# Performance work log

Hardware: AMD Instinct MI355X
Metric: run time of the kernel (lower is better)

The kernel has to match this reference:

```python
import jax, jax.numpy as jnp
import numpy as np


def setup_inputs() -> dict:
    key = jax.random.key(0)
    k1, k2, k3, k4, k5 = jax.random.split(key, 5)
    B, Tx, Ty, E, D = 8, 256, 256, 256, 256
    return {
        "encoder_out_seq": jax.random.normal(k1, (B, Tx, E), dtype=jnp.float32),
        "decoder_out_seq": jax.random.normal(k2, (B, Ty, D), dtype=jnp.float32),
        "W_a": jax.random.normal(k3, (E, E), dtype=jnp.float32) * 0.05,
        "U_a": jax.random.normal(k4, (D, E), dtype=jnp.float32) * 0.05,
        "V_a": jax.random.normal(k5, (E, 1), dtype=jnp.float32) * 0.05,
    }


def reference(encoder_out_seq, decoder_out_seq, W_a, U_a, V_a):
    # encoder_out_seq: [B, Tx, E], decoder_out_seq: [B, Ty, D]
    # Vectorized Bahdanau additive attention (the K.rnn scan is a fake
    # recurrence: each timestep only uses the per-step decoder input and the
    # constant encoder sequence).
    W_dot_s = jnp.einsum("bxe,ef->bxf", encoder_out_seq, W_a)   # [B, Tx, E]
    U_dot_h = jnp.einsum("byd,de->bye", decoder_out_seq, U_a)   # [B, Ty, E]
    # [B, Ty, Tx, E] broadcast add + tanh, then project with V_a -> [B, Ty, Tx]
    Ws_plus_Uh = jnp.tanh(W_dot_s[:, None, :, :] + U_dot_h[:, :, None, :])
    e = jnp.einsum("byxe,eo->byx", Ws_plus_Uh, V_a)             # [B, Ty, Tx]
    e = jax.nn.softmax(e, axis=-1)                               # softmax over Tx
    # context: weighted sum of encoder states -> [B, Ty, E]
    c = jnp.einsum("byx,bxe->bye", e, encoder_out_seq)
    return (c, e)
```

## Files before the change

### kernel.cpp

```cpp
#include <hip/hip_runtime.h>
#include <cstddef>
#include <stdint.h>

#define NB 8
#define TX 256
#define TY 256
#define NE 256

#define CSC 2.8853900817779268f

__global__ __launch_bounds__(512) void prep_kernel(
    const float* __restrict__ enc, const float* __restrict__ dec,
    const float* __restrict__ Wa, const float* __restrict__ Ua,
    float* __restrict__ ZwT, float* __restrict__ Zu)
{
    const int tx = threadIdx.x;
    const int w  = threadIdx.y;
    const int tid = w * 64 + tx;
    int blk = blockIdx.x;
    const bool isU = blk >= 128;
    if (isU) blk -= 128;
    const int b  = blk >> 4;
    const int r0 = (blk & 15) * 16;

    __shared__ float rowsL[16 * NE];
    __shared__ float tL[16][260];

    const float* src = (isU ? dec : enc) + ((size_t)b * 256 + r0) * NE;
    ((float4*)rowsL)[tid]       = ((const float4*)src)[tid];
    ((float4*)rowsL)[tid + 512] = ((const float4*)src)[tid + 512];
    __syncthreads();

    const float* M = isU ? Ua : Wa;
    const int e0 = tx * 4;
    const int rA = w * 2, rB = w * 2 + 1;
    float4 acc0 = make_float4(0.f, 0.f, 0.f, 0.f);
    float4 acc1 = make_float4(0.f, 0.f, 0.f, 0.f);
    const float* rowA = rowsL + rA * NE;
    const float* rowB = rowsL + rB * NE;

    for (int k = 0; k < NE; k += 8) {
        float4 mw[8];
        #pragma unroll
        for (int j = 0; j < 8; ++j)
            mw[j] = *(const float4*)(M + (size_t)(k + j) * NE + e0);
        #pragma unroll
        for (int j = 0; j < 8; ++j) {
            const float a = rowA[k + j];
            const float c = rowB[k + j];
            acc0.x = __builtin_fmaf(a, mw[j].x, acc0.x);
            acc0.y = __builtin_fmaf(a, mw[j].y, acc0.y);
            acc0.z = __builtin_fmaf(a, mw[j].z, acc0.z);
            acc0.w = __builtin_fmaf(a, mw[j].w, acc0.w);
            acc1.x = __builtin_fmaf(c, mw[j].x, acc1.x);
            acc1.y = __builtin_fmaf(c, mw[j].y, acc1.y);
            acc1.z = __builtin_fmaf(c, mw[j].z, acc1.z);
            acc1.w = __builtin_fmaf(c, mw[j].w, acc1.w);
        }
    }
    acc0.x = __builtin_amdgcn_exp2f(acc0.x * CSC);
    acc0.y = __builtin_amdgcn_exp2f(acc0.y * CSC);
    acc0.z = __builtin_amdgcn_exp2f(acc0.z * CSC);
    acc0.w = __builtin_amdgcn_exp2f(acc0.w * CSC);
    acc1.x = __builtin_amdgcn_exp2f(acc1.x * CSC);
    acc1.y = __builtin_amdgcn_exp2f(acc1.y * CSC);
    acc1.z = __builtin_amdgcn_exp2f(acc1.z * CSC);
    acc1.w = __builtin_amdgcn_exp2f(acc1.w * CSC);

    if (isU) {
        *(float4*)(Zu + ((size_t)b * TY + r0 + rA) * NE + e0) = acc0;
        *(float4*)(Zu + ((size_t)b * TY + r0 + rB) * NE + e0) = acc1;
    } else {
        *(float4*)&tL[rA][e0] = acc0;
        *(float4*)&tL[rB][e0] = acc1;
        __syncthreads();
        #pragma unroll
        for (int rep = 0; rep < 2; ++rep) {
            const int f4id = tid + rep * 512;
            const int e  = f4id >> 2;
            const int xq = (f4id & 3) * 4;
            float4 o;
            o.x = tL[xq + 0][e];
            o.y = tL[xq + 1][e];
            o.z = tL[xq + 2][e];
            o.w = tL[xq + 3][e];
            *(float4*)(ZwT + (size_t)b * NE * TX + (size_t)e * TX + r0 + xq) = o;
        }
    }
}

__global__ __launch_bounds__(512, 4) void attn_kernel(
    const float* __restrict__ enc, const float* __restrict__ ZwT,
    const float* __restrict__ Zu, const float* __restrict__ Va,
    float* __restrict__ c_out, float* __restrict__ e_out)
{
    const int tx = threadIdx.x;
    const int w  = threadIdx.y;
    const int tid = w * 64 + tx;
    const int b  = blockIdx.x & 7;
    const int y0 = (blockIdx.x >> 3) * 4;

    __shared__ float4 zu4L[NE];
    __shared__ float  vL[NE];
    __shared__ float4 accL[8][4][64];
    __shared__ float  pL4[TX][4];

    {
        const int e = tid & 255;
        if (tid < 256) {
            const float* zp = Zu + ((size_t)b * TY + y0) * NE + e;
            zu4L[e] = make_float4(zp[0], zp[NE], zp[2 * NE], zp[3 * NE]);
        } else {
            vL[e] = Va[e];
        }
    }
    __syncthreads();

    const float* wp = ZwT + (size_t)b * NE * TX + (size_t)(w * 32) * TX + tx * 4;
    const float4* zup = &zu4L[w * 32];
    const float*  vp  = &vL[w * 32];
    float4 acc0 = make_float4(0.f, 0.f, 0.f, 0.f);
    float4 acc1 = acc0, acc2 = acc0, acc3 = acc0;
    #pragma unroll 4
    for (int e = 0; e < 32; ++e) {
        const float4 zw  = *(const float4*)(wp + (size_t)e * TX);
        const float4 zu4 = zup[e];
        const float  v   = vp[e];
        acc0.x = __builtin_fmaf(v, __builtin_amdgcn_rcpf(__builtin_fmaf(zw.x, zu4.x, 1.f)), acc0.x);
        acc0.y = __builtin_fmaf(v, __builtin_amdgcn_rcpf(__builtin_fmaf(zw.y, zu4.x, 1.f)), acc0.y);
        acc0.z = __builtin_fmaf(v, __builtin_amdgcn_rcpf(__builtin_fmaf(zw.z, zu4.x, 1.f)), acc0.z);
        acc0.w = __builtin_fmaf(v, __builtin_amdgcn_rcpf(__builtin_fmaf(zw.w, zu4.x, 1.f)), acc0.w);
        acc1.x = __builtin_fmaf(v, __builtin_amdgcn_rcpf(__builtin_fmaf(zw.x, zu4.y, 1.f)), acc1.x);
        acc1.y = __builtin_fmaf(v, __builtin_amdgcn_rcpf(__builtin_fmaf(zw.y, zu4.y, 1.f)), acc1.y);
        acc1.z = __builtin_fmaf(v, __builtin_amdgcn_rcpf(__builtin_fmaf(zw.z, zu4.y, 1.f)), acc1.z);
        acc1.w = __builtin_fmaf(v, __builtin_amdgcn_rcpf(__builtin_fmaf(zw.w, zu4.y, 1.f)), acc1.w);
        acc2.x = __builtin_fmaf(v, __builtin_amdgcn_rcpf(__builtin_fmaf(zw.x, zu4.z, 1.f)), acc2.x);
        acc2.y = __builtin_fmaf(v, __builtin_amdgcn_rcpf(__builtin_fmaf(zw.y, zu4.z, 1.f)), acc2.y);
        acc2.z = __builtin_fmaf(v, __builtin_amdgcn_rcpf(__builtin_fmaf(zw.z, zu4.z, 1.f)), acc2.z);
        acc2.w = __builtin_fmaf(v, __builtin_amdgcn_rcpf(__builtin_fmaf(zw.w, zu4.z, 1.f)), acc2.w);
        acc3.x = __builtin_fmaf(v, __builtin_amdgcn_rcpf(__builtin_fmaf(zw.x, zu4.w, 1.f)), acc3.x);
        acc3.y = __builtin_fmaf(v, __builtin_amdgcn_rcpf(__builtin_fmaf(zw.y, zu4.w, 1.f)), acc3.y);
        acc3.z = __builtin_fmaf(v, __builtin_amdgcn_rcpf(__builtin_fmaf(zw.z, zu4.w, 1.f)), acc3.z);
        acc3.w = __builtin_fmaf(v, __builtin_amdgcn_rcpf(__builtin_fmaf(zw.w, zu4.w, 1.f)), acc3.w);
    }
    accL[w][0][tx] = acc0;
    accL[w][1][tx] = acc1;
    accL[w][2][tx] = acc2;
    accL[w][3][tx] = acc3;
    __syncthreads();

    const int yy = w & 3;
    float4 s = make_float4(0.f, 0.f, 0.f, 0.f);
    #pragma unroll
    for (int ww = 0; ww < 8; ++ww) {
        const float4 a = accL[ww][yy][tx];
        s.x += a.x; s.y += a.y; s.z += a.z; s.w += a.w;
    }
    s.x *= -2.f; s.y *= -2.f; s.z *= -2.f; s.w *= -2.f;

    float m = fmaxf(fmaxf(s.x, s.y), fmaxf(s.z, s.w));
    #pragma unroll
    for (int off = 32; off; off >>= 1) m = fmaxf(m, __shfl_xor(m, off));
    float4 p;
    p.x = __expf(s.x - m);
    p.y = __expf(s.y - m);
    p.z = __expf(s.z - m);
    p.w = __expf(s.w - m);
    float sum = (p.x + p.y) + (p.z + p.w);
    #pragma unroll
    for (int off = 32; off; off >>= 1) sum += __shfl_xor(sum, off);
    const float inv = __builtin_amdgcn_rcpf(sum);
    p.x *= inv; p.y *= inv; p.z *= inv; p.w *= inv;

    if (w < 4) {
        *(float4*)(e_out + ((size_t)b * TY + y0 + yy) * TX + tx * 4) = p;
        pL4[tx * 4 + 0][yy] = p.x;
        pL4[tx * 4 + 1][yy] = p.y;
        pL4[tx * 4 + 2][yy] = p.z;
        pL4[tx * 4 + 3][yy] = p.w;
    }
    __syncthreads();

    const float* ep = enc + (size_t)b * TX * NE + (size_t)(w * 32) * NE + tx * 4;
    float4 c0 = make_float4(0.f, 0.f, 0.f, 0.f);
    float4 c1 = c0, c2 = c0, c3 = c0;
    #pragma unroll 4
    for (int x = 0; x < 32; ++x) {
        const float4 ev = *(const float4*)(ep + (size_t)x * NE);
        const float4 p4 = *(const float4*)&pL4[w * 32 + x][0];
        c0.x = __builtin_fmaf(p4.x, ev.x, c0.x);
        c0.y = __builtin_fmaf(p4.x, ev.y, c0.y);
        c0.z = __builtin_fmaf(p4.x, ev.z, c0.z);
        c0.w = __builtin_fmaf(p4.x, ev.w, c0.w);
        c1.x = __builtin_fmaf(p4.y, ev.x, c1.x);
        c1.y = __builtin_fmaf(p4.y, ev.y, c1.y);
        c1.z = __builtin_fmaf(p4.y, ev.z, c1.z);
        c1.w = __builtin_fmaf(p4.y, ev.w, c1.w);
        c2.x = __builtin_fmaf(p4.z, ev.x, c2.x);
        c2.y = __builtin_fmaf(p4.z, ev.y, c2.y);
        c2.z = __builtin_fmaf(p4.z, ev.z, c2.z);
        c2.w = __builtin_fmaf(p4.z, ev.w, c2.w);
        c3.x = __builtin_fmaf(p4.w, ev.x, c3.x);
        c3.y = __builtin_fmaf(p4.w, ev.y, c3.y);
        c3.z = __builtin_fmaf(p4.w, ev.z, c3.z);
        c3.w = __builtin_fmaf(p4.w, ev.w, c3.w);
    }
    __syncthreads();
    accL[w][0][tx] = c0;
    accL[w][1][tx] = c1;
    accL[w][2][tx] = c2;
    accL[w][3][tx] = c3;
    __syncthreads();

    if (w < 4) {
        float4 cs = make_float4(0.f, 0.f, 0.f, 0.f);
        #pragma unroll
        for (int ww = 0; ww < 8; ++ww) {
            const float4 t = accL[ww][w][tx];
            cs.x += t.x; cs.y += t.y; cs.z += t.z; cs.w += t.w;
        }
        *(float4*)(c_out + ((size_t)b * TY + y0 + w) * NE + tx * 4) = cs;
    }
}

extern "C" void kernel_launch(void* const* d_in, const int* in_sizes, int n_in,
                              void* d_out, int out_size, void* d_ws, size_t ws_size,
                              hipStream_t stream) {
    const float* enc = (const float*)d_in[0];
    const float* dec = (const float*)d_in[1];
    const float* Wa  = (const float*)d_in[2];
    const float* Ua  = (const float*)d_in[3];
    const float* Va  = (const float*)d_in[4];

    float* c_out = (float*)d_out;
    float* e_out = (float*)d_out + (size_t)NB * TY * NE;

    float* ZwT = (float*)d_ws;
    float* Zu  = (float*)d_ws + (size_t)NB * NE * TX;

    prep_kernel<<<256, dim3(64, 8), 0, stream>>>(enc, dec, Wa, Ua, ZwT, Zu);
    attn_kernel<<<512, dim3(64, 8), 0, stream>>>(enc, ZwT, Zu, Va, c_out, e_out);
}
```

Before: 43.01 us.

## Stage projection weights through double-buffered LDS with async global-to-LDS loads

The prep projection kernel now copies 16-row chunks of the weight matrix into a double-buffered shared-memory area using global_load_lds. The next chunk is prefetched while the current one is consumed, and a barrier closes each chunk. Before, every wave read the full weight matrix from global memory on its own. This cuts redundant global/L2 traffic and overlaps loads with FMAs, at the cost of about 32KB more LDS and 16 barriers per block. It relies on __syncthreads waiting for the outstanding async LDS loads.

```diff
diff --git a/kernel.cpp b/kernel.cpp
--- a/kernel.cpp
+++ b/kernel.cpp
@@ -8,6 +8,13 @@
 #define NE 256
 
 #define CSC 2.8853900817779268f
+
+__device__ __forceinline__ void gload_lds16(const float* g, float* l) {
+    __builtin_amdgcn_global_load_lds(
+        (const __attribute__((address_space(1))) void*)g,
+        (__attribute__((address_space(3))) void*)l,
+        16, 0, 0);
+}
 
 __global__ __launch_bounds__(512) void prep_kernel(
     const float* __restrict__ enc, const float* __restrict__ dec,
@@ -24,14 +31,18 @@
     const int r0 = (blk & 15) * 16;
 
     __shared__ float rowsL[16 * NE];
+    __shared__ float MbL[2][16 * NE];
     __shared__ float tL[16][260];
 
+    const float* M = isU ? Ua : Wa;
+
+    gload_lds16(M + tid * 4,        MbL[0] + w * 256);
+    gload_lds16(M + 2048 + tid * 4, MbL[0] + 2048 + w * 256);
     const float* src = (isU ? dec : enc) + ((size_t)b * 256 + r0) * NE;
     ((float4*)rowsL)[tid]       = ((const float4*)src)[tid];
     ((float4*)rowsL)[tid + 512] = ((const float4*)src)[tid + 512];
     __syncthreads();
 
-    const float* M = isU ? Ua : Wa;
     const int e0 = tx * 4;
     const int rA = w * 2, rB = w * 2 + 1;
     float4 acc0 = make_float4(0.f, 0.f, 0.f, 0.f);
@@ -39,25 +50,32 @@
     const float* rowA = rowsL + rA * NE;
     const float* rowB = rowsL + rB * NE;
 
-    for (int k = 0; k < NE; k += 8) {
-        float4 mw[8];
+    for (int c = 0; c < 16; ++c) {
+        if (c < 15) {
+            const float* g = M + (size_t)(c + 1) * 4096;
+            float* dst = MbL[(c + 1) & 1];
+            gload_lds16(g + tid * 4,        dst + w * 256);
+            gload_lds16(g + 2048 + tid * 4, dst + 2048 + w * 256);
+        }
+        const float* mb = MbL[c & 1] + e0;
+        const int kbase = c * 16;
         #pragma unroll
-        for (int j = 0; j < 8; ++j)
-            mw[j] = *(const float4*)(M + (size_t)(k + j) * NE + e0);
-        #pragma unroll
-        for (int j = 0; j < 8; ++j) {
-            const float a = rowA[k + j];
-            const float c = rowB[k + j];
-            acc0.x = __builtin_fmaf(a, mw[j].x, acc0.x);
-            acc0.y = __builtin_fmaf(a, mw[j].y, acc0.y);
-            acc0.z = __builtin_fmaf(a, mw[j].z, acc0.z);
-            acc0.w = __builtin_fmaf(a, mw[j].w, acc0.w);
-            acc1.x = __builtin_fmaf(c, mw[j].x, acc1.x);
-            acc1.y = __builtin_fmaf(c, mw[j].y, acc1.y);
-            acc1.z = __builtin_fmaf(c, mw[j].z, acc1.z);
-            acc1.w = __builtin_fmaf(c, mw[j].w, acc1.w);
-        }
-    }
+        for (int j = 0; j < 16; ++j) {
+            const float4 mw = *(const float4*)(mb + j * NE);
+            const float a = rowA[kbase + j];
+            const float d = rowB[kbase + j];
+            acc0.x = __builtin_fmaf(a, mw.x, acc0.x);
+            acc0.y = __builtin_fmaf(a, mw.y, acc0.y);
+            acc0.z = __builtin_fmaf(a, mw.z, acc0.z);
+            acc0.w = __builtin_fmaf(a, mw.w, acc0.w);
+            acc1.x = __builtin_fmaf(d, mw.x, acc1.x);
+            acc1.y = __builtin_fmaf(d, mw.y, acc1.y);
+            acc1.z = __builtin_fmaf(d, mw.z, acc1.z);
+            acc1.w = __builtin_fmaf(d, mw.w, acc1.w);
+        }
+        __syncthreads();
+    }
+
     acc0.x = __builtin_amdgcn_exp2f(acc0.x * CSC);
     acc0.y = __builtin_amdgcn_exp2f(acc0.y * CSC);
     acc0.z = __builtin_amdgcn_exp2f(acc0.z * CSC);
```

Measured after the change: 39.61 us. 1.09x faster.

## Split prep GEMM along K across lanes with shuffle reduction and more blocks

Applied to the files above, without the earlier changes.

The projection prep kernel is restructured. It now launches 1024 blocks of 256 threads, each computing a 16-row by 64-column tile. Within a wave the K dimension is split across 16 lane groups, each accumulating 16 rows of partial sums, followed by an xor-shuffle reduction. Inputs are staged transposed in LDS, with register prefetch of the next weight and row values. This raises parallelism and occupancy for the small GEMM, at the cost of many shuffle instructions and high register use for the 64-float accumulator array.

```diff
diff --git a/kernel.cpp b/kernel.cpp
--- a/kernel.cpp
+++ b/kernel.cpp
@@ -9,83 +9,114 @@
 
 #define CSC 2.8853900817779268f
 
-__global__ __launch_bounds__(512) void prep_kernel(
+__global__ __launch_bounds__(256, 4) void prep_kernel(
     const float* __restrict__ enc, const float* __restrict__ dec,
     const float* __restrict__ Wa, const float* __restrict__ Ua,
     float* __restrict__ ZwT, float* __restrict__ Zu)
 {
-    const int tx = threadIdx.x;
-    const int w  = threadIdx.y;
+    const int tx  = threadIdx.x;
+    const int w   = threadIdx.y;
     const int tid = w * 64 + tx;
     int blk = blockIdx.x;
-    const bool isU = blk >= 128;
-    if (isU) blk -= 128;
-    const int b  = blk >> 4;
-    const int r0 = (blk & 15) * 16;
-
-    __shared__ float rowsL[16 * NE];
-    __shared__ float tL[16][260];
-
-    const float* src = (isU ? dec : enc) + ((size_t)b * 256 + r0) * NE;
-    ((float4*)rowsL)[tid]       = ((const float4*)src)[tid];
-    ((float4*)rowsL)[tid + 512] = ((const float4*)src)[tid + 512];
-    __syncthreads();
-
+    const bool isU = blk >= 512;
+    if (isU) blk -= 512;
+    const int rowTile = blk >> 2;
+    const int c0      = (blk & 3) * 64;
+    const int R       = rowTile * 16;
+    const int b       = R >> 8;
+    const int rloc    = R & 255;
+
+    __shared__ float rowsT[256][20];
+    __shared__ float tL[16][68];
+
+    const float* src = (isU ? dec : enc) + (size_t)R * NE;
+    #pragma unroll
+    for (int j = 0; j < 4; ++j) {
+        const int f   = tid + j * 256;
+        const int row = f & 15;
+        const int kq  = f >> 4;
+        const float4 v = ((const float4*)src)[row * 64 + kq];
+        rowsT[kq * 4 + 0][row] = v.x;
+        rowsT[kq * 4 + 1][row] = v.y;
+        rowsT[kq * 4 + 2][row] = v.z;
+        rowsT[kq * 4 + 3][row] = v.w;
+    }
+    __syncthreads();
+
+    const int cq = tx & 3;
+    const int kp = tx >> 2;
     const float* M = isU ? Ua : Wa;
-    const int e0 = tx * 4;
-    const int rA = w * 2, rB = w * 2 + 1;
-    float4 acc0 = make_float4(0.f, 0.f, 0.f, 0.f);
-    float4 acc1 = make_float4(0.f, 0.f, 0.f, 0.f);
-    const float* rowA = rowsL + rA * NE;
-    const float* rowB = rowsL + rB * NE;
-
-    for (int k = 0; k < NE; k += 8) {
-        float4 mw[8];
+    const float* mp = M + (size_t)kp * NE + (c0 + w * 16 + cq * 4);
+
+    float4 acc[16];
+    #pragma unroll
+    for (int r = 0; r < 16; ++r) acc[r] = make_float4(0.f, 0.f, 0.f, 0.f);
+
+    float4 mw  = *(const float4*)mp;
+    float4 rv0 = *(const float4*)&rowsT[kp][0];
+    float4 rv1 = *(const float4*)&rowsT[kp][4];
+    float4 rv2 = *(const float4*)&rowsT[kp][8];
+    float4 rv3 = *(const float4*)&rowsT[kp][12];
+
+#define ACC4(A, S) \
+    A.x = __builtin_fmaf(S, mc.x, A.x); \
+    A.y = __builtin_fmaf(S, mc.y, A.y); \
+    A.z = __builtin_fmaf(S, mc.z, A.z); \
+    A.w = __builtin_fmaf(S, mc.w, A.w);
+
+    #pragma unroll
+    for (int t = 0; t < 16; ++t) {
+        const float4 mc = mw;
+        const float4 a0 = rv0, a1 = rv1, a2 = rv2, a3 = rv3;
+        if (t < 15) {
+            mp += 16 * NE;
+            mw = *(const float4*)mp;
+            const int kn = (t + 1) * 16 + kp;
+            rv0 = *(const float4*)&rowsT[kn][0];
+            rv1 = *(const float4*)&rowsT[kn][4];
+            rv2 = *(const float4*)&rowsT[kn][8];
+            rv3 = *(const float4*)&rowsT[kn][12];
+        }
+        ACC4(acc[0],  a0.x) ACC4(acc[1],  a0.y) ACC4(acc[2],  a0.z) ACC4(acc[3],  a0.w)
+        ACC4(acc[4],  a1.x) ACC4(acc[5],  a1.y) ACC4(acc[6],  a1.z) ACC4(acc[7],  a1.w)
+        ACC4(acc[8],  a2.x) ACC4(acc[9],  a2.y) ACC4(acc[10], a2.z) ACC4(acc[11], a2.w)
+        ACC4(acc[12], a3.x) ACC4(acc[13], a3.y) ACC4(acc[14], a3.z) ACC4(acc[15], a3.w)
+    }
+#undef ACC4
+
+    #pragma unroll
+    for (int off = 4; off <= 32; off <<= 1) {
         #pragma unroll
-        for (int j = 0; j < 8; ++j)
-            mw[j] = *(const float4*)(M + (size_t)(k + j) * NE + e0);
-        #pragma unroll
-        for (int j = 0; j < 8; ++j) {
-            const float a = rowA[k + j];
-            const float c = rowB[k + j];
-            acc0.x = __builtin_fmaf(a, mw[j].x, acc0.x);
-            acc0.y = __builtin_fmaf(a, mw[j].y, acc0.y);
-            acc0.z = __builtin_fmaf(a, mw[j].z, acc0.z);
-            acc0.w = __builtin_fmaf(a, mw[j].w, acc0.w);
-            acc1.x = __builtin_fmaf(c, mw[j].x, acc1.x);
-            acc1.y = __builtin_fmaf(c, mw[j].y, acc1.y);
-            acc1.z = __builtin_fmaf(c, mw[j].z, acc1.z);
-            acc1.w = __builtin_fmaf(c, mw[j].w, acc1.w);
-        }
-    }
-    acc0.x = __builtin_amdgcn_exp2f(acc0.x * CSC);
-    acc0.y = __builtin_amdgcn_exp2f(acc0.y * CSC);
-    acc0.z = __builtin_amdgcn_exp2f(acc0.z * CSC);
-    acc0.w = __builtin_amdgcn_exp2f(acc0.w * CSC);
-    acc1.x = __builtin_amdgcn_exp2f(acc1.x * CSC);
-    acc1.y = __builtin_amdgcn_exp2f(acc1.y * CSC);
-    acc1.z = __builtin_amdgcn_exp2f(acc1.z * CSC);
-    acc1.w = __builtin_amdgcn_exp2f(acc1.w * CSC);
+        for (int r = 0; r < 16; ++r) {
+            acc[r].x += __shfl_xor(acc[r].x, off);
+            acc[r].y += __shfl_xor(acc[r].y, off);
+            acc[r].z += __shfl_xor(acc[r].z, off);
+            acc[r].w += __shfl_xor(acc[r].w, off);
+        }
+    }
+
+    float4 o = acc[0];
+    #pragma unroll
+    for (int r = 1; r < 16; ++r) if (kp == r) o = acc[r];
+
+    o.x = __builtin_amdgcn_exp2f(o.x * CSC);
+    o.y = __builtin_amdgcn_exp2f(o.y * CSC);
+    o.z = __builtin_amdgcn_exp2f(o.z * CSC);
+    o.w = __builtin_amdgcn_exp2f(o.w * CSC);
 
     if (isU) {
-        *(float4*)(Zu + ((size_t)b * TY + r0 + rA) * NE + e0) = acc0;
-        *(float4*)(Zu + ((size_t)b * TY + r0 + rB) * NE + e0) = acc1;
+        *(float4*)(Zu + ((size_t)b * TY + rloc + kp) * NE + c0 + w * 16 + cq * 4) = o;
     } else {
-        *(float4*)&tL[rA][e0] = acc0;
-        *(float4*)&tL[rB][e0] = acc1;
+        *(float4*)&tL[kp][w * 16 + cq * 4] = o;
         __syncthreads();
-        #pragma unroll
-        for (int rep = 0; rep < 2; ++rep) {
-            const int f4id = tid + rep * 512;
-            const int e  = f4id >> 2;
-            const int xq = (f4id & 3) * 4;
-            float4 o;
-            o.x = tL[xq + 0][e];
-            o.y = tL[xq + 1][e];
-            o.z = tL[xq + 2][e];
-            o.w = tL[xq + 3][e];
-            *(float4*)(ZwT + (size_t)b * NE * TX + (size_t)e * TX + r0 + xq) = o;
-        }
+        const int ee = tid >> 2;
+        const int xq = tid & 3;
+        float4 o2;
+        o2.x = tL[xq * 4 + 0][ee];
+        o2.y = tL[xq * 4 + 1][ee];
+        o2.z = tL[xq * 4 + 2][ee];
+        o2.w = tL[xq * 4 + 3][ee];
+        *(float4*)(ZwT + ((size_t)b * NE + c0 + ee) * TX + rloc + xq * 4) = o2;
     }
 }
 
@@ -238,6 +269,6 @@
     float* ZwT = (float*)d_ws;
     float* Zu  = (float*)d_ws + (size_t)NB * NE * TX;
 
-    prep_kernel<<<256, dim3(64, 8), 0, stream>>>(enc, dec, Wa, Ua, ZwT, Zu);
+    prep_kernel<<<1024, dim3(64, 4), 0, stream>>>(enc, dec, Wa, Ua, ZwT, Zu);
     attn_kernel<<<512, dim3(64, 8), 0, stream>>>(enc, ZwT, Zu, Va, c_out, e_out);
 }
```

Result: slower. 48.57 us (+12.9%).
